# Kernel tuning notes

Hardware: AMD Instinct MI355X
Metric: run time of the kernel (lower is better)

## Reference

```python
import jax, jax.numpy as jnp
import numpy as np

ROWS, COLS, CH = 16, 16, 3
HID, HEADS, BLEN = 512, 8, 128
NUM_POINTS = ROWS * COLS            # 256
SEQ = ROWS * COLS * CH              # 768
NF = 256
L = 6
EPS = 1e-6


def setup_inputs() -> dict:
    key = jax.random.key(0)
    ks = jax.random.split(key, 16)
    w = 0.02  # keep logits in a sane range
    return {
        "X": jax.random.uniform(ks[0], (16, CH, ROWS, COLS), jnp.float32),
        "embed_table": jax.random.normal(ks[1], (NUM_POINTS * CH, HID), jnp.float32) * w,
        "Wq": jax.random.normal(ks[2], (L, HID, HID), jnp.float32) * w,
        "Wk": jax.random.normal(ks[3], (L, HID, HID), jnp.float32) * w,
        "Wv": jax.random.normal(ks[4], (L, HID, HID), jnp.float32) * w,
        "Wo": jax.random.normal(ks[5], (L, HID, HID), jnp.float32) * w,
        "ln1_g": jnp.ones((L, HID), jnp.float32),
        "ln1_b": jnp.zeros((L, HID), jnp.float32),
        "W1": jax.random.normal(ks[6], (L, HID, 4 * HID), jnp.float32) * w,
        "b1": jnp.zeros((L, 4 * HID), jnp.float32),
        "W2": jax.random.normal(ks[7], (L, 4 * HID, HID), jnp.float32) * w,
        "b2": jnp.zeros((L, HID), jnp.float32),
        "ln2_g": jnp.ones((L, HID), jnp.float32),
        "ln2_b": jnp.zeros((L, HID), jnp.float32),
        "proj_W": jax.random.normal(ks[8], (HID * SEQ, NF), jnp.float32) * w,
        "out_ln_g": jnp.ones((NF,), jnp.float32),
        "out_ln_b": jnp.zeros((NF,), jnp.float32),
    }


def _ln(x, g, b):
    m = jnp.mean(x, axis=-1, keepdims=True)
    v = jnp.mean(jnp.square(x - m), axis=-1, keepdims=True)
    return (x - m) * jax.lax.rsqrt(v + EPS) * g + b


def _timing_signal(x4):
    # x4: [B, ROWS, COLS*CH, HID]; 2 spatial dims
    nts = HID // 4
    inv = jnp.exp(jnp.arange(nts, dtype=jnp.float32) * (-np.log(10000.0) / (nts - 1)))
    def sig(length, prepad, postpad):
        pos = jnp.arange(length, dtype=jnp.float32)
        st = pos[:, None] * inv[None, :]
        s = jnp.concatenate([jnp.sin(st), jnp.cos(st)], axis=1)  # [len, 2*nts]
        return jnp.pad(s, ((0, 0), (prepad, postpad)))
    s0 = sig(x4.shape[1], 0, HID - 2 * nts)          # dim 0 (rows)
    s1 = sig(x4.shape[2], 2 * nts, 0)                # dim 1 (cols*ch)
    return x4 + s0[None, :, None, :] + s1[None, None, :, :]


def _local_attn(x, wq, wk, wv, wo):
    B, S, _ = x.shape
    dh = HID // HEADS
    def heads(w):
        return (x @ w).reshape(B, S, HEADS, dh).transpose(0, 2, 1, 3)
    q = heads(wq) * (dh ** -0.5)
    k = heads(wk)
    v = heads(wv)
    nb = S // BLEN  # S is a multiple of BLEN here (768/128=6), so no padding
    neg = jnp.float32(-1e9)
    bias1 = neg * jnp.triu(jnp.ones((BLEN, BLEN), jnp.float32), 1)
    logits1 = jnp.einsum('bhkd,bhqd->bhqk', k[:, :, :BLEN], q[:, :, :BLEN]) + bias1
    first = jax.nn.softmax(logits1, axis=-1) @ v[:, :, :BLEN]  # [B,H,BLEN,dh]
    qb = q.reshape(B, HEADS, nb, BLEN, dh)
    kb = k.reshape(B, HEADS, nb, BLEN, dh)
    vb = v.reshape(B, HEADS, nb, BLEN, dh)
    lk = jnp.concatenate([kb[:, :, :-1], kb[:, :, 1:]], axis=3)  # [B,H,nb-1,2B,dh]
    lv = jnp.concatenate([vb[:, :, :-1], vb[:, :, 1:]], axis=3)
    tq = qb[:, :, 1:]
    bias2 = neg * jnp.triu(jnp.ones((BLEN, 2 * BLEN), jnp.float32), BLEN + 1)
    logits2 = jnp.einsum('bhnkd,bhnqd->bhnqk', lk, tq) + bias2
    tail = jnp.einsum('bhnqk,bhnkd->bhnqd', jax.nn.softmax(logits2, axis=-1), lv)
    tail = tail.reshape(B, HEADS, (nb - 1) * BLEN, dh)
    out = jnp.concatenate([first, tail], axis=2)  # [B,H,S,dh]
    out = out.transpose(0, 2, 1, 3).reshape(B, S, HID)
    return out @ wo


def reference(X, embed_table, Wq, Wk, Wv, Wo, ln1_g, ln1_b, W1, b1, W2, b2,
              ln2_g, ln2_b, proj_W, out_ln_g, out_ln_b):
    B = X.shape[0]
    # [B,C,H,W] -> [B,H,W,C] -> [B,H,W*C]
    x = X.transpose(0, 2, 3, 1).reshape(B, ROWS, COLS * CH)
    idx = (x * (NUM_POINTS - 1)).astype(jnp.int32)
    chan_add = jnp.tile(jnp.arange(CH, dtype=jnp.int32) * NUM_POINTS, COLS)  # [W*C]
    idx = idx + chan_add[None, None, :]
    e = embed_table[idx] * (HID ** 0.5)             # [B,H,W*C,HID]
    # shift_and_pad over flattened spatial dims
    flat = e.reshape(B, SEQ, HID)
    flat = jnp.pad(flat[:, :-1], ((0, 0), (1, 0), (0, 0)))
    e = flat.reshape(B, ROWS, COLS * CH, HID)
    e = _timing_signal(e)
    h = e.reshape(B, SEQ, HID)
    for i in range(L):
        y = _local_attn(h, Wq[i], Wk[i], Wv[i], Wo[i])
        h = _ln(y + h, ln1_g[i], ln1_b[i])
        y = jax.nn.gelu(h @ W1[i] + b1[i], approximate=False) @ W2[i] + b2[i]
        h = _ln(y + h, ln2_g[i], ln2_b[i])
    out = h.reshape(B, SEQ * HID) @ proj_W
    out = jax.nn.gelu(out, approximate=False)
    return _ln(out, out_ln_g, out_ln_b)
```

## Files before the change

### kernel.cpp

```cpp
#include <hip/hip_runtime.h>
#include <cstddef>

typedef __bf16 bf16;
typedef bf16 bf16x4 __attribute__((ext_vector_type(4)));
typedef bf16 bf16x8 __attribute__((ext_vector_type(8)));
typedef float f32x4 __attribute__((ext_vector_type(4)));

#define NLAYER 6
#define HIDD 512
#define SEQL 768
#define NBATCH 16
#define MROWS 12288
#define QKVS 1536

__device__ __forceinline__ void gll16(const void* g, void* l) {
  __builtin_amdgcn_global_load_lds((const __attribute__((address_space(1))) void*)g,
                                   (__attribute__((address_space(3))) void*)l, 16, 0, 0);
}

__device__ __forceinline__ float gelu_f(float v) {
  return 0.5f * v * (1.0f + erff(v * 0.7071067811865475f));
}

#define VMC8 asm volatile("s_waitcnt vmcnt(8)" ::: "memory");
#define VMC4 asm volatile("s_waitcnt vmcnt(4)" ::: "memory");
#define VMC0 asm volatile("s_waitcnt vmcnt(0)" ::: "memory");

__global__ __launch_bounds__(256) void prep(
    const float* __restrict__ X, const float* __restrict__ ET,
    const float* __restrict__ Wq, const float* __restrict__ Wk,
    const float* __restrict__ Wv, const float* __restrict__ Wo,
    const float* __restrict__ W1, const float* __restrict__ W2,
    const float* __restrict__ ln1g, const float* __restrict__ ln1b,
    const float* __restrict__ ln2g, const float* __restrict__ ln2b,
    bf16* __restrict__ Wqkvt, bf16* __restrict__ Wot,
    bf16* __restrict__ W1t, bf16* __restrict__ W2t,
    float* __restrict__ vQg, float* __restrict__ vQb,
    float* __restrict__ vW1g, float* __restrict__ vW1b,
    bf16* __restrict__ Zg2) {
  const int bx = blockIdx.x;
  const int t = threadIdx.x;
  if (bx < 18432) {
    const int l = bx / 3072, idx = bx % 3072;
    const float* src;
    bf16* dst;
    int K, N, kb, nb;
    if (idx < 1024) {
      const int which = idx >> 8, tile = idx & 255;
      nb = (tile & 15) * 32; kb = (tile >> 4) * 32; K = 512; N = 512;
      const float* s4[4] = {Wq, Wk, Wv, Wo};
      src = s4[which] + (size_t)l * 512 * 512;
      dst = (which < 3) ? (Wqkvt + (size_t)l * QKVS * 512 + (size_t)which * 512 * 512)
                        : (Wot + (size_t)l * 512 * 512);
    } else if (idx < 2048) {
      const int local = idx - 1024;
      nb = (local & 63) * 32; kb = (local >> 6) * 32; K = 512; N = 2048;
      src = W1 + (size_t)l * 512 * 2048; dst = W1t + (size_t)l * 512 * 2048;
    } else {
      const int local = idx - 2048;
      nb = (local & 15) * 32; kb = (local >> 4) * 32; K = 2048; N = 512;
      src = W2 + (size_t)l * 2048 * 512; dst = W2t + (size_t)l * 2048 * 512;
    }
    __shared__ float tile[32 * 33];
#pragma unroll
    for (int i = 0; i < 4; ++i) {
      int lin = i * 256 + t, r = lin >> 5, c = lin & 31;
      tile[r * 33 + c] = src[(size_t)(kb + r) * N + nb + c];
    }
    __syncthreads();
#pragma unroll
    for (int i = 0; i < 4; ++i) {
      int lin = i * 256 + t, r = lin >> 5, c = lin & 31;
      dst[(size_t)(nb + r) * K + kb + c] = (bf16)tile[c * 33 + r];
    }
    return;
  }
  if (bx < 18432 + 84) {
    const int i = bx - 18432;
    const int l = i / 14;
    const int c = (i % 14) * 256 + t;
    if (c < 1536) {
      float gv = 0.f, bv = 0.f;
      if (l > 0) {
        const float* gin = ln2g + (l - 1) * 512;
        const float* bin = ln2b + (l - 1) * 512;
        const float* W;
        int cc = c;
        if (c < 512) { W = Wq + (size_t)l * 512 * 512; }
        else if (c < 1024) { W = Wk + (size_t)l * 512 * 512; cc = c - 512; }
        else { W = Wv + (size_t)l * 512 * 512; cc = c - 1024; }
        for (int k = 0; k < 512; ++k) {
          const float w = W[(size_t)k * 512 + cc];
          gv += gin[k] * w;
          bv += bin[k] * w;
        }
      }
      vQg[l * 1536 + c] = gv;
      vQb[l * 1536 + c] = bv;
    } else {
      const int cc = c - 1536;
      const float* g1 = ln1g + l * 512;
      const float* b1 = ln1b + l * 512;
      const float* W = W1 + (size_t)l * 512 * 2048;
      float gv = 0.f, bv = 0.f;
      for (int k = 0; k < 512; ++k) {
        const float w = W[(size_t)k * 2048 + cc];
        gv += g1[k] * w;
        bv += b1[k] * w;
      }
      vW1g[l * 2048 + cc] = gv;
      vW1b[l * 2048 + cc] = bv;
    }
    return;
  }
  const int bs = (bx - 18516) * 2 + (t >> 7);
  const int tl = t & 127;
  const int s = bs % SEQL;
  const int b = bs / SEQL;
  const int r = s / 48, c = s % 48;
  float vals[4] = {0.f, 0.f, 0.f, 0.f};
  const int ssrc = s - 1;
  if (ssrc >= 0) {
    const int rs = ssrc / 48, c48 = ssrc % 48;
    const int col = c48 / 3, ch = c48 % 3;
    const float x = X[((b * 3 + ch) * 16 + rs) * 16 + col];
    const int idx = (int)(x * 255.0f) + ch * 256;
    const float sq = 22.62741699796952f;
#pragma unroll
    for (int i = 0; i < 4; ++i) vals[i] = ET[(size_t)idx * HIDD + tl + 128 * i] * sq;
  }
  const float Cc = -0.07252236513366286f;
#pragma unroll
  for (int i = 0; i < 4; ++i) {
    const int d = tl + 128 * i;
    float ts;
    if (d < 128)      ts = sinf((float)r * expf((float)d * Cc));
    else if (d < 256) ts = cosf((float)r * expf((float)(d - 128) * Cc));
    else if (d < 384) ts = sinf((float)c * expf((float)(d - 256) * Cc));
    else              ts = cosf((float)c * expf((float)(d - 384) * Cc));
    Zg2[(size_t)bs * HIDD + d] = (bf16)(vals[i] + ts);
  }
}

template <int EPI, bool L0, int KT>
__global__ __launch_bounds__(256) void gemm2p(const bf16* __restrict__ A,
                                              const bf16* __restrict__ Bt,
                                              bf16* __restrict__ C,
                                              bf16* __restrict__ vT,
                                              const float* __restrict__ pIn,
                                              const float* __restrict__ vg,
                                              const float* __restrict__ vb,
                                              const float* __restrict__ bias,
                                              int N) {
  constexpr int K = KT;
  constexpr int NI = K >> 5;
  __shared__ char sbuf[49152];
  __shared__ float rsL[128], rsmL[128];
  const int tid = threadIdx.x;
  const int lane = tid & 63, w = tid >> 6;
  const int wr = w >> 1, wc = w & 1;
  const int l15 = lane & 15, g = lane >> 4;
  const int m0 = blockIdx.y * 128, n0 = blockIdx.x * 128;
  f32x4 acc[4][4] = {};
  const int rr0 = tid >> 2, kc = tid & 3;
  const bf16* Ap0 = A + (size_t)(m0 + rr0) * K + kc * 8;
  const bf16* Ap1 = A + (size_t)(m0 + 64 + rr0) * K + kc * 8;
  const bf16* Bp0 = Bt + (size_t)(n0 + rr0) * K + kc * 8;
  const bf16* Bp1 = Bt + (size_t)(n0 + 64 + rr0) * K + kc * 8;

  auto STAGE = [&](int st, int kt) {
    char* base = sbuf + st * 16384;
    gll16(Ap0 + kt, base + tid * 16);
    gll16(Ap1 + kt, base + 4096 + tid * 16);
    gll16(Bp0 + kt, base + 8192 + tid * 16);
    gll16(Bp1 + kt, base + 12288 + tid * 16);
  };

  STAGE(0, 0);
  STAGE(1, 32);
#pragma unroll 3
  for (int it = 0; it < NI; ++it) {
    const int cur = it % 3;
    if (it + 2 < NI) {
      STAGE((it + 2) % 3, (it + 2) * 32);
      VMC8;
    } else if (it + 1 < NI) {
      VMC4;
    } else {
      VMC0;
    }
    __builtin_amdgcn_s_barrier();
    const char* base = sbuf + cur * 16384;
    bf16x8 af[4], bv[4];
#pragma unroll
    for (int i = 0; i < 4; ++i)
      af[i] = *(const bf16x8*)(base + ((wr * 64 + i * 16 + l15) * 32 + 8 * g) * 2);
#pragma unroll
    for (int i = 0; i < 4; ++i)
      bv[i] = *(const bf16x8*)(base + 8192 + ((wc * 64 + i * 16 + l15) * 32 + 8 * g) * 2);
#pragma unroll
    for (int mi = 0; mi < 4; ++mi)
#pragma unroll
      for (int ni = 0; ni < 4; ++ni)
        acc[mi][ni] = __builtin_amdgcn_mfma_f32_16x16x32_bf16(af[mi], bv[ni], acc[mi][ni], 0, 0, 0);
    __builtin_amdgcn_s_barrier();
  }

  if constexpr (!L0) {
    if (tid < 128) {
      const int row = m0 + tid;
      float s = 0.f, q = 0.f;
#pragma unroll
      for (int j = 0; j < 8; ++j) {
        s += pIn[(size_t)j * MROWS + row];
        q += pIn[(size_t)(8 + j) * MROWS + row];
      }
      const float mean = s * (1.0f / 512.0f);
      const float var = q * (1.0f / 512.0f) - mean * mean;
      const float rs = rsqrtf(var + 1e-6f);
      rsL[tid] = rs;
      rsmL[tid] = rs * mean;
    }
    __syncthreads();
  }

  const bool VPATH = (EPI == 0) && (n0 >= 1024);
#pragma unroll
  for (int mi = 0; mi < 4; ++mi)
#pragma unroll
    for (int nf = 0; nf < 4; ++nf) {
      const int lr = wr * 64 + mi * 16 + 4 * g;
      const int row = m0 + lr;
      const int col = n0 + wc * 64 + nf * 16 + l15;
      float vgc = 0.f, vbc = 0.f, bc = 0.f;
      if constexpr (!L0) { vgc = vg[col]; vbc = vb[col]; }
      if constexpr (EPI == 1) bc = bias[col];
      float val[4];
#pragma unroll
      for (int r = 0; r < 4; ++r) {
        float a = acc[mi][nf][r];
        float v;
        if constexpr (L0) v = a;
        else v = rsL[lr + r] * a - rsmL[lr + r] * vgc + vbc;
        if constexpr (EPI == 1) v = gelu_f(v + bc);
        val[r] = v;
      }
      if (VPATH) {
        const int cv = col - 1024, hh = cv >> 6, dd = cv & 63;
        const int b = row / SEQL, s = row % SEQL;
        bf16x4 q4;
#pragma unroll
        for (int r = 0; r < 4; ++r) q4[r] = (bf16)val[r];
        *(bf16x4*)&vT[(size_t)((b * 8 + hh) * 64 + dd) * SEQL + s] = q4;
      } else {
#pragma unroll
        for (int r = 0; r < 4; ++r)
          C[(size_t)(row + r) * N + col] = (bf16)val[r];
      }
    }
}

template <int EPI, int KT>
__global__ __launch_bounds__(256) void gemm_fuse(const bf16* __restrict__ A,
                                                 const bf16* __restrict__ Bt,
                                                 const bf16* __restrict__ zgIn,
                                                 const float* __restrict__ pIn,
                                                 const float* __restrict__ vg_in,
                                                 const float* __restrict__ vb_in,
                                                 const float* __restrict__ extra_b,
                                                 const float* __restrict__ g_out,
                                                 bf16* __restrict__ zgOut,
                                                 float* __restrict__ pOut) {
  constexpr int N = 512;
  constexpr int K = KT;
  constexpr int NI = K >> 5;
  __shared__ char sbuf[49152];
  __shared__ float rsL[128], rsmL[128];
  const int tid = threadIdx.x;
  const int lane = tid & 63, w = tid >> 6;
  const int wr = w >> 1, wc = w & 1;
  const int l15 = lane & 15, g = lane >> 4;
  const int m0 = blockIdx.y * 128, n0 = blockIdx.x * 128;
  f32x4 acc[4][4] = {};
  const int rr0 = tid >> 2, kc = tid & 3;
  const bf16* Ap0 = A + (size_t)(m0 + rr0) * K + kc * 8;
  const bf16* Ap1 = A + (size_t)(m0 + 64 + rr0) * K + kc * 8;
  const bf16* Bp0 = Bt + (size_t)(n0 + rr0) * K + kc * 8;
  const bf16* Bp1 = Bt + (size_t)(n0 + 64 + rr0) * K + kc * 8;

  auto STAGE = [&](int st, int kt) {
    char* base = sbuf + st * 16384;
    gll16(Ap0 + kt, base + tid * 16);
    gll16(Ap1 + kt, base + 4096 + tid * 16);
    gll16(Bp0 + kt, base + 8192 + tid * 16);
    gll16(Bp1 + kt, base + 12288 + tid * 16);
  };

  STAGE(0, 0);
  STAGE(1, 32);
#pragma unroll 3
  for (int it = 0; it < NI; ++it) {
    const int cur = it % 3;
    if (it + 2 < NI) {
      STAGE((it + 2) % 3, (it + 2) * 32);
      VMC8;
    } else if (it + 1 < NI) {
      VMC4;
    } else {
      VMC0;
    }
    __builtin_amdgcn_s_barrier();
    const char* base = sbuf + cur * 16384;
    bf16x8 af[4], bv[4];
#pragma unroll
    for (int i = 0; i < 4; ++i)
      af[i] = *(const bf16x8*)(base + ((wr * 64 + i * 16 + l15) * 32 + 8 * g) * 2);
#pragma unroll
    for (int i = 0; i < 4; ++i)
      bv[i] = *(const bf16x8*)(base + 8192 + ((wc * 64 + i * 16 + l15) * 32 + 8 * g) * 2);
#pragma unroll
    for (int mi = 0; mi < 4; ++mi)
#pragma unroll
      for (int ni = 0; ni < 4; ++ni)
        acc[mi][ni] = __builtin_amdgcn_mfma_f32_16x16x32_bf16(af[mi], bv[ni], acc[mi][ni], 0, 0, 0);
    __builtin_amdgcn_s_barrier();
  }

  bf16* ztile = (bf16*)sbuf;
#pragma unroll
  for (int j = 0; j < 8; ++j) {
    const int row = j * 16 + (tid >> 4);
    const bf16* gsrc = zgIn + (size_t)(m0 + row) * N + n0 + (tid & 15) * 8;
    gll16(gsrc, sbuf + j * 4096 + tid * 16);
  }

  if constexpr (EPI != 0) {
    if (tid < 128) {
      const int row = m0 + tid;
      float s = 0.f, q = 0.f;
#pragma unroll
      for (int j = 0; j < 8; ++j) {
        s += pIn[(size_t)j * MROWS + row];
        q += pIn[(size_t)(8 + j) * MROWS + row];
      }
      const float mean = s * (1.0f / 512.0f);
      const float var = q * (1.0f / 512.0f) - mean * mean;
      const float rs = rsqrtf(var + 1e-6f);
      rsL[tid] = rs;
      rsmL[tid] = rs * mean;
    }
  }
  VMC0;
  __syncthreads();

  const int nb = n0 >> 7;
  float vgc[4], vbc[4], go[4], eb[4];
#pragma unroll
  for (int ni = 0; ni < 4; ++ni) {
    const int col = n0 + wc * 64 + ni * 16 + l15;
    if constexpr (EPI != 0) { vgc[ni] = vg_in[col]; vbc[ni] = vb_in[col]; }
    go[ni] = g_out[col];
    if constexpr (EPI == 2) eb[ni] = extra_b[col];
  }
#pragma unroll
  for (int mi = 0; mi < 4; ++mi) {
#pragma unroll
    for (int rr = 0; rr < 4; ++rr) {
      const int lr = wr * 64 + mi * 16 + 4 * g + rr;
      const int row = m0 + lr;
      float s = 0.f, q = 0.f;
#pragma unroll
      for (int ni = 0; ni < 4; ++ni) {
        const int lc = wc * 64 + ni * 16 + l15;
        const float zgv = (float)ztile[lr * 128 + lc];
        float hprev;
        if constexpr (EPI == 0) hprev = zgv;
        else hprev = rsL[lr] * zgv - rsmL[lr] * vgc[ni] + vbc[ni];
        float z = acc[mi][ni][rr] + hprev;
        if constexpr (EPI == 2) z += eb[ni];
        s += z;
        q += z * z;
        ztile[lr * 128 + lc] = (bf16)(z * go[ni]);
      }
      s += __shfl_xor(s, 1); s += __shfl_xor(s, 2); s += __shfl_xor(s, 4); s += __shfl_xor(s, 8);
      q += __shfl_xor(q, 1); q += __shfl_xor(q, 2); q += __shfl_xor(q, 4); q += __shfl_xor(q, 8);
      if (l15 == 0) {
        pOut[(size_t)(nb * 2 + wc) * MROWS + row] = s;
        pOut[(size_t)(8 + nb * 2 + wc) * MROWS + row] = q;
      }
    }
  }
  __syncthreads();
#pragma unroll
  for (int i = 0; i < 8; ++i) {
    const int id = i * 256 + tid;
    const int row = id >> 4, c16 = id & 15;
    bf16x8 v = *(const bf16x8*)&ztile[row * 128 + c16 * 8];
    *(bf16x8*)&zgOut[(size_t)(m0 + row) * N + n0 + c16 * 8] = v;
  }
}

template <bool FIRST>
__device__ __forceinline__ void attn_body(int n, int h, int b, const bf16* __restrict__ Qb,
                                          const bf16* __restrict__ Kb,
                                          const bf16* __restrict__ Vt,
                                          bf16* __restrict__ O, bf16* __restrict__ P) {
  constexpr int NF = FIRST ? 8 : 16;
  constexpr int KC = FIRST ? 4 : 8;
  const int tid = threadIdx.x, w = tid >> 6, lane = tid & 63;
  const int l15 = lane & 15, g = lane >> 4;
  const int keybase = FIRST ? 0 : (n - 1) * 128;
  const int qbase = n * 128;
  const bf16* qrow = Qb + (size_t)(b * SEQL + qbase + w * 16 + l15) * QKVS + h * 64;
  bf16x8 qf0 = *(const bf16x8*)(qrow + 8 * g);
  bf16x8 qf1 = *(const bf16x8*)(qrow + 32 + 8 * g);
  f32x4 S[NF];
#pragma unroll
  for (int nf = 0; nf < NF; ++nf) S[nf] = f32x4{0.f, 0.f, 0.f, 0.f};
#pragma unroll
  for (int nf = 0; nf < NF; ++nf) {
    const bf16* krow = Kb + (size_t)(b * SEQL + keybase + nf * 16 + l15) * QKVS + h * 64;
    bf16x8 kf0 = *(const bf16x8*)(krow + 8 * g);
    bf16x8 kf1 = *(const bf16x8*)(krow + 32 + 8 * g);
    S[nf] = __builtin_amdgcn_mfma_f32_16x16x32_bf16(qf0, kf0, S[nf], 0, 0, 0);
    S[nf] = __builtin_amdgcn_mfma_f32_16x16x32_bf16(qf1, kf1, S[nf], 0, 0, 0);
  }
#pragma unroll
  for (int rr = 0; rr < 4; ++rr) {
    const int qloc = w * 16 + 4 * g + rr;
    float mx = -3.0e38f;
#pragma unroll
    for (int nf = 0; nf < NF; ++nf) {
      const int key = nf * 16 + l15;
      const bool valid = FIRST ? (key <= qloc) : (key <= qloc + 128);
      float v = valid ? S[nf][rr] * 0.125f : -1.0e9f;
      S[nf][rr] = v;
      mx = fmaxf(mx, v);
    }
    mx = fmaxf(mx, __shfl_xor(mx, 1));
    mx = fmaxf(mx, __shfl_xor(mx, 2));
    mx = fmaxf(mx, __shfl_xor(mx, 4));
    mx = fmaxf(mx, __shfl_xor(mx, 8));
    float sden = 0.f;
#pragma unroll
    for (int nf = 0; nf < NF; ++nf) {
      float e = expf(S[nf][rr] - mx);
      S[nf][rr] = e;
      sden += e;
    }
    sden += __shfl_xor(sden, 1);
    sden += __shfl_xor(sden, 2);
    sden += __shfl_xor(sden, 4);
    sden += __shfl_xor(sden, 8);
    const float rcp = 1.0f / sden;
#pragma unroll
    for (int nf = 0; nf < NF; ++nf)
      P[w * 4096 + (4 * g + rr) * 256 + nf * 16 + l15] = (bf16)(S[nf][rr] * rcp);
  }
  f32x4 Oacc[4];
#pragma unroll
  for (int i = 0; i < 4; ++i) Oacc[i] = f32x4{0.f, 0.f, 0.f, 0.f};
#pragma unroll
  for (int kc = 0; kc < KC; ++kc) {
    bf16x8 pa = *(const bf16x8*)&P[w * 4096 + l15 * 256 + kc * 32 + 8 * g];
#pragma unroll
    for (int nf = 0; nf < 4; ++nf) {
      const bf16* vrow = Vt + (size_t)((b * 8 + h) * 64 + nf * 16 + l15) * SEQL +
                         keybase + kc * 32 + 8 * g;
      bf16x8 vf = *(const bf16x8*)vrow;
      Oacc[nf] = __builtin_amdgcn_mfma_f32_16x16x32_bf16(pa, vf, Oacc[nf], 0, 0, 0);
    }
  }
  bf16* Ow = P + w * 4096;
#pragma unroll
  for (int nf = 0; nf < 4; ++nf)
#pragma unroll
    for (int rr = 0; rr < 4; ++rr)
      Ow[(4 * g + rr) * 68 + nf * 16 + l15] = (bf16)Oacc[nf][rr];
#pragma unroll
  for (int i = 0; i < 2; ++i) {
    const int id = i * 64 + lane;
    const int row = id >> 3, c8 = id & 7;
    bf16x8 v = *(const bf16x8*)&Ow[row * 68 + c8 * 8];
    *(bf16x8*)&O[(size_t)(b * SEQL + qbase + w * 16 + row) * HIDD + h * 64 + c8 * 8] = v;
  }
}

__global__ __launch_bounds__(512) void attn_all(const bf16* __restrict__ Qb,
                                                const bf16* __restrict__ Kb,
                                                const bf16* __restrict__ Vt,
                                                bf16* __restrict__ O) {
  __shared__ bf16 P[8 * 4096];
  const int n = blockIdx.x, h = blockIdx.y, b = blockIdx.z;
  if (n == 0)
    attn_body<true>(0, h, b, Qb, Kb, Vt, O, P);
  else
    attn_body<false>(n, h, b, Qb, Kb, Vt, O, P);
}

__global__ __launch_bounds__(256) void proj_partial(const bf16* __restrict__ zg2,
                                                    const float* __restrict__ pSQ2,
                                                    const float* __restrict__ g5,
                                                    const float* __restrict__ b5,
                                                    const float* __restrict__ W,
                                                    float* __restrict__ part) {
  const int kc = blockIdx.x;
  const int t = threadIdx.x;
  __shared__ float Al[512 * 20];
  __shared__ float gld[512], bld[512], rsP[16], rsmP[16];
  gld[t] = g5[t]; gld[t + 256] = g5[t + 256];
  bld[t] = b5[t]; bld[t + 256] = b5[t + 256];
  if (t < 16) {
    const int row = t * SEQL + kc;
    float s = 0.f, q = 0.f;
#pragma unroll
    for (int j = 0; j < 8; ++j) {
      s += pSQ2[(size_t)j * MROWS + row];
      q += pSQ2[(size_t)(8 + j) * MROWS + row];
    }
    const float mean = s * (1.0f / 512.0f);
    const float var = q * (1.0f / 512.0f) - mean * mean;
    const float rs = rsqrtf(var + 1e-6f);
    rsP[t] = rs;
    rsmP[t] = rs * mean;
  }
  __syncthreads();
#pragma unroll
  for (int i = 0; i < 32; ++i) {
    int lin = i * 256 + t, m = lin >> 9, kk = lin & 511;
    const int row = m * SEQL + kc;
    Al[kk * 20 + m] = rsP[m] * (float)zg2[(size_t)row * 512 + kk] - rsmP[m] * gld[kk] + bld[kk];
  }
  __syncthreads();
  const size_t k0 = (size_t)kc * 512;
  float acc[16] = {};
  for (int kk = 0; kk < 512; ++kk) {
    const float wv = W[(k0 + kk) * 256 + t];
    const f32x4* a = (const f32x4*)&Al[kk * 20];
#pragma unroll
    for (int j = 0; j < 4; ++j) {
      f32x4 av = a[j];
      acc[j * 4 + 0] += av[0] * wv;
      acc[j * 4 + 1] += av[1] * wv;
      acc[j * 4 + 2] += av[2] * wv;
      acc[j * 4 + 3] += av[3] * wv;
    }
  }
#pragma unroll
  for (int m = 0; m < 16; ++m) part[(size_t)kc * 4096 + m * 256 + t] = acc[m];
}

__global__ __launch_bounds__(256) void proj_reduce1(const float* __restrict__ part,
                                                    float* __restrict__ part2) {
  const int i = blockIdx.x * 256 + threadIdx.x;
  const int cb = blockIdx.y;
  float s = 0.f;
  for (int c = cb * 64; c < cb * 64 + 64; ++c) s += part[(size_t)c * 4096 + i];
  part2[(size_t)cb * 4096 + i] = s;
}

__global__ __launch_bounds__(256) void proj_final(const float* __restrict__ part2,
                                                  const float* __restrict__ g,
                                                  const float* __restrict__ bt,
                                                  float* __restrict__ out) {
  const int row = blockIdx.x, t = threadIdx.x;
  float v = 0.f;
#pragma unroll
  for (int c = 0; c < 12; ++c) v += part2[(size_t)c * 4096 + row * 256 + t];
  const float x = gelu_f(v);
  __shared__ float red[256];
  red[t] = x;
  __syncthreads();
  for (int off = 128; off > 0; off >>= 1) {
    if (t < off) red[t] += red[t + off];
    __syncthreads();
  }
  const float mean = red[0] * (1.0f / 256.0f);
  __syncthreads();
  const float dx = x - mean;
  red[t] = dx * dx;
  __syncthreads();
  for (int off = 128; off > 0; off >>= 1) {
    if (t < off) red[t] += red[t + off];
    __syncthreads();
  }
  const float var = red[0] * (1.0f / 256.0f);
  const float rs = rsqrtf(var + 1e-6f);
  out[row * 256 + t] = dx * rs * g[t] + bt[t];
}

extern "C" void kernel_launch(void* const* d_in, const int* in_sizes, int n_in,
                              void* d_out, int out_size, void* d_ws, size_t ws_size,
                              hipStream_t stream) {
  const float* X = (const float*)d_in[0];
  const float* ET = (const float*)d_in[1];
  const float* Wq = (const float*)d_in[2];
  const float* Wk = (const float*)d_in[3];
  const float* Wv = (const float*)d_in[4];
  const float* Wo = (const float*)d_in[5];
  const float* ln1g = (const float*)d_in[6];
  const float* ln1b = (const float*)d_in[7];
  const float* W1 = (const float*)d_in[8];
  const float* b1 = (const float*)d_in[9];
  const float* W2 = (const float*)d_in[10];
  const float* b2 = (const float*)d_in[11];
  const float* ln2g = (const float*)d_in[12];
  const float* ln2b = (const float*)d_in[13];
  const float* PW = (const float*)d_in[14];
  const float* og = (const float*)d_in[15];
  const float* obv = (const float*)d_in[16];
  float* out = (float*)d_out;

  char* p = (char*)d_ws;
  auto alloc = [&](size_t bytes) {
    char* r = p;
    p += (bytes + 255) & ~(size_t)255;
    return r;
  };
  bf16* Wqkvt = (bf16*)alloc((size_t)NLAYER * QKVS * 512 * 2);
  bf16* Wot = (bf16*)alloc((size_t)NLAYER * 512 * 512 * 2);
  bf16* W1t = (bf16*)alloc((size_t)NLAYER * 512 * 2048 * 2);
  bf16* W2t = (bf16*)alloc((size_t)NLAYER * 512 * 2048 * 2);
  float* vQg = (float*)alloc((size_t)NLAYER * QKVS * 4);
  float* vQb = (float*)alloc((size_t)NLAYER * QKVS * 4);
  float* vW1g = (float*)alloc((size_t)NLAYER * 2048 * 4);
  float* vW1b = (float*)alloc((size_t)NLAYER * 2048 * 4);
  bf16* zg2 = (bf16*)alloc((size_t)MROWS * HIDD * 2);
  bf16* zg1 = (bf16*)alloc((size_t)MROWS * HIDD * 2);
  float* pSQ1 = (float*)alloc((size_t)16 * MROWS * 4);
  float* pSQ2 = (float*)alloc((size_t)16 * MROWS * 4);
  bf16* qkvB = (bf16*)alloc((size_t)MROWS * QKVS * 2);
  bf16* vT = (bf16*)alloc((size_t)MROWS * HIDD * 2);
  bf16* aO = (bf16*)alloc((size_t)MROWS * HIDD * 2);
  bf16* mid = (bf16*)alloc((size_t)MROWS * 2048 * 2);
  float* part = (float*)alloc((size_t)768 * 4096 * 4);
  float* part2 = (float*)alloc((size_t)12 * 4096 * 4);
  (void)ws_size; (void)n_in; (void)in_sizes; (void)out_size;

  prep<<<24660, 256, 0, stream>>>(X, ET, Wq, Wk, Wv, Wo, W1, W2, ln1g, ln1b, ln2g, ln2b,
                                  Wqkvt, Wot, W1t, W2t, vQg, vQb, vW1g, vW1b, zg2);

  for (int i = 0; i < NLAYER; ++i) {
    const bf16* WqkvL = Wqkvt + (size_t)i * QKVS * 512;
    const bf16* WoL = Wot + (size_t)i * 512 * 512;
    const bf16* W1L = W1t + (size_t)i * 512 * 2048;
    const bf16* W2L = W2t + (size_t)i * 512 * 2048;
    if (i == 0)
      gemm2p<0, true, 512><<<dim3(12, 96), 256, 0, stream>>>(zg2, WqkvL, qkvB, vT, pSQ2,
                                                             vQg, vQb, nullptr, QKVS);
    else
      gemm2p<0, false, 512><<<dim3(12, 96), 256, 0, stream>>>(zg2, WqkvL, qkvB, vT, pSQ2,
                                                              vQg + i * QKVS, vQb + i * QKVS,
                                                              nullptr, QKVS);
    attn_all<<<dim3(6, 8, 16), 512, 0, stream>>>(qkvB, qkvB + 512, vT, aO);
    if (i == 0)
      gemm_fuse<0, 512><<<dim3(4, 96), 256, 0, stream>>>(aO, WoL, zg2, nullptr, nullptr,
                                                         nullptr, nullptr, ln1g, zg1, pSQ1);
    else
      gemm_fuse<1, 512><<<dim3(4, 96), 256, 0, stream>>>(aO, WoL, zg2, pSQ2,
                                                         ln2g + (i - 1) * 512,
                                                         ln2b + (i - 1) * 512, nullptr,
                                                         ln1g + i * 512, zg1, pSQ1);
    gemm2p<1, false, 512><<<dim3(16, 96), 256, 0, stream>>>(zg1, W1L, mid, nullptr, pSQ1,
                                                            vW1g + i * 2048, vW1b + i * 2048,
                                                            b1 + i * 2048, 2048);
    gemm_fuse<2, 2048><<<dim3(4, 96), 256, 0, stream>>>(mid, W2L, zg1, pSQ1, ln1g + i * 512,
                                                        ln1b + i * 512, b2 + i * 512,
                                                        ln2g + i * 512, zg2, pSQ2);
  }

  proj_partial<<<768, 256, 0, stream>>>(zg2, pSQ2, ln2g + 5 * 512, ln2b + 5 * 512, PW, part);
  proj_reduce1<<<dim3(16, 12), 256, 0, stream>>>(part, part2);
  proj_final<<<16, 256, 0, stream>>>(part2, og, obv, out);
}
```

Before: 1.434 ms.

## Stage K and V tiles in swizzled LDS for local attention

Attention blocks now bulk-load the K and V tiles for their key window into LDS with global_load_lds, using an XOR swizzle. All 8 waves then read those tiles from LDS instead of each wave fetching the same K/V rows from global memory. Probabilities are kept in registers and written to LDS one 32-key chunk at a time, and O is stored directly from the accumulators. Launch bounds now request 4 waves per SIMD. Shared memory per block grows to about 74KB, which may limit occupancy, and the direct O stores are narrower.

```diff
diff --git a/kernel.cpp b/kernel.cpp
--- a/kernel.cpp
+++ b/kernel.cpp
@@ -400,28 +400,55 @@
   }
 }
 
-template <bool FIRST>
-__device__ __forceinline__ void attn_body(int n, int h, int b, const bf16* __restrict__ Qb,
+template <int NKEY>
+__device__ __forceinline__ void attn_body(int n, int h, int b,
+                                          const bf16* __restrict__ Qb,
                                           const bf16* __restrict__ Kb,
                                           const bf16* __restrict__ Vt,
-                                          bf16* __restrict__ O, bf16* __restrict__ P) {
-  constexpr int NF = FIRST ? 8 : 16;
-  constexpr int KC = FIRST ? 4 : 8;
+                                          bf16* __restrict__ O,
+                                          bf16* __restrict__ Ks,
+                                          bf16* __restrict__ Vs,
+                                          bf16* __restrict__ Pc) {
+  constexpr int NF = NKEY / 16;
+  constexpr int KC = NKEY / 32;
+  constexpr int VG = NKEY / 8;
   const int tid = threadIdx.x, w = tid >> 6, lane = tid & 63;
   const int l15 = lane & 15, g = lane >> 4;
-  const int keybase = FIRST ? 0 : (n - 1) * 128;
+  const int keybase = (NKEY == 128) ? 0 : (n - 1) * 128;
   const int qbase = n * 128;
+
+#pragma unroll
+  for (int p = 0; p < NKEY / 64; ++p) {
+    const int j = p * 512 + tid;
+    const int row = j >> 3, lg = j & 7;
+    const int pg = lg ^ (row & 7);
+    gll16(Kb + (size_t)(b * SEQL + keybase + row) * QKVS + h * 64 + pg * 8, Ks + j * 8);
+  }
+#pragma unroll
+  for (int p = 0; p < NKEY / 64; ++p) {
+    const int j = p * 512 + tid;
+    const int row = j / VG, lg = j % VG;
+    const int pg = lg ^ (row & (VG - 1));
+    gll16(Vt + (size_t)((b * 8 + h) * 64 + row) * SEQL + keybase + pg * 8, Vs + j * 8);
+  }
+
   const bf16* qrow = Qb + (size_t)(b * SEQL + qbase + w * 16 + l15) * QKVS + h * 64;
   bf16x8 qf0 = *(const bf16x8*)(qrow + 8 * g);
   bf16x8 qf1 = *(const bf16x8*)(qrow + 32 + 8 * g);
+
+  VMC0;
+  __syncthreads();
+
   f32x4 S[NF];
 #pragma unroll
   for (int nf = 0; nf < NF; ++nf) S[nf] = f32x4{0.f, 0.f, 0.f, 0.f};
 #pragma unroll
   for (int nf = 0; nf < NF; ++nf) {
-    const bf16* krow = Kb + (size_t)(b * SEQL + keybase + nf * 16 + l15) * QKVS + h * 64;
-    bf16x8 kf0 = *(const bf16x8*)(krow + 8 * g);
-    bf16x8 kf1 = *(const bf16x8*)(krow + 32 + 8 * g);
+    const int krow = nf * 16 + l15;
+    const int pg0 = g ^ (krow & 7);
+    const int pg1 = (g + 4) ^ (krow & 7);
+    bf16x8 kf0 = *(const bf16x8*)&Ks[krow * 64 + pg0 * 8];
+    bf16x8 kf1 = *(const bf16x8*)&Ks[krow * 64 + pg1 * 8];
     S[nf] = __builtin_amdgcn_mfma_f32_16x16x32_bf16(qf0, kf0, S[nf], 0, 0, 0);
     S[nf] = __builtin_amdgcn_mfma_f32_16x16x32_bf16(qf1, kf1, S[nf], 0, 0, 0);
   }
@@ -432,7 +459,7 @@
 #pragma unroll
     for (int nf = 0; nf < NF; ++nf) {
       const int key = nf * 16 + l15;
-      const bool valid = FIRST ? (key <= qloc) : (key <= qloc + 128);
+      const bool valid = (NKEY == 128) ? (key <= qloc) : (key <= qloc + 128);
       float v = valid ? S[nf][rr] * 0.125f : -1.0e9f;
       S[nf][rr] = v;
       mx = fmaxf(mx, v);
@@ -454,48 +481,49 @@
     sden += __shfl_xor(sden, 8);
     const float rcp = 1.0f / sden;
 #pragma unroll
-    for (int nf = 0; nf < NF; ++nf)
-      P[w * 4096 + (4 * g + rr) * 256 + nf * 16 + l15] = (bf16)(S[nf][rr] * rcp);
-  }
+    for (int nf = 0; nf < NF; ++nf) S[nf][rr] *= rcp;
+  }
+
+  bf16* pcw = Pc + w * 640;
   f32x4 Oacc[4];
 #pragma unroll
   for (int i = 0; i < 4; ++i) Oacc[i] = f32x4{0.f, 0.f, 0.f, 0.f};
 #pragma unroll
   for (int kc = 0; kc < KC; ++kc) {
-    bf16x8 pa = *(const bf16x8*)&P[w * 4096 + l15 * 256 + kc * 32 + 8 * g];
+#pragma unroll
+    for (int rr = 0; rr < 4; ++rr) {
+      pcw[(4 * g + rr) * 40 + l15] = (bf16)S[2 * kc][rr];
+      pcw[(4 * g + rr) * 40 + 16 + l15] = (bf16)S[2 * kc + 1][rr];
+    }
+    bf16x8 pa = *(const bf16x8*)&pcw[l15 * 40 + 8 * g];
 #pragma unroll
     for (int nf = 0; nf < 4; ++nf) {
-      const bf16* vrow = Vt + (size_t)((b * 8 + h) * 64 + nf * 16 + l15) * SEQL +
-                         keybase + kc * 32 + 8 * g;
-      bf16x8 vf = *(const bf16x8*)vrow;
+      const int vrow = nf * 16 + l15;
+      const int pg = (kc * 4 + g) ^ (vrow & (VG - 1));
+      bf16x8 vf = *(const bf16x8*)&Vs[vrow * NKEY + pg * 8];
       Oacc[nf] = __builtin_amdgcn_mfma_f32_16x16x32_bf16(pa, vf, Oacc[nf], 0, 0, 0);
     }
   }
-  bf16* Ow = P + w * 4096;
 #pragma unroll
   for (int nf = 0; nf < 4; ++nf)
 #pragma unroll
     for (int rr = 0; rr < 4; ++rr)
-      Ow[(4 * g + rr) * 68 + nf * 16 + l15] = (bf16)Oacc[nf][rr];
-#pragma unroll
-  for (int i = 0; i < 2; ++i) {
-    const int id = i * 64 + lane;
-    const int row = id >> 3, c8 = id & 7;
-    bf16x8 v = *(const bf16x8*)&Ow[row * 68 + c8 * 8];
-    *(bf16x8*)&O[(size_t)(b * SEQL + qbase + w * 16 + row) * HIDD + h * 64 + c8 * 8] = v;
-  }
-}
-
-__global__ __launch_bounds__(512) void attn_all(const bf16* __restrict__ Qb,
-                                                const bf16* __restrict__ Kb,
-                                                const bf16* __restrict__ Vt,
-                                                bf16* __restrict__ O) {
-  __shared__ bf16 P[8 * 4096];
+      O[(size_t)(b * SEQL + qbase + w * 16 + 4 * g + rr) * HIDD + h * 64 + nf * 16 + l15] =
+          (bf16)Oacc[nf][rr];
+}
+
+__global__ __launch_bounds__(512, 4) void attn_all(const bf16* __restrict__ Qb,
+                                                   const bf16* __restrict__ Kb,
+                                                   const bf16* __restrict__ Vt,
+                                                   bf16* __restrict__ O) {
+  __shared__ bf16 Ks[256 * 64];
+  __shared__ bf16 Vs[64 * 256];
+  __shared__ bf16 Pc[8 * 640];
   const int n = blockIdx.x, h = blockIdx.y, b = blockIdx.z;
   if (n == 0)
-    attn_body<true>(0, h, b, Qb, Kb, Vt, O, P);
+    attn_body<128>(0, h, b, Qb, Kb, Vt, O, Ks, Vs, Pc);
   else
-    attn_body<false>(n, h, b, Qb, Kb, Vt, O, P);
+    attn_body<256>(n, h, b, Qb, Kb, Vt, O, Ks, Vs, Pc);
 }
 
 __global__ __launch_bounds__(256) void proj_partial(const bf16* __restrict__ zg2,
```

Result: faster. 1.246 ms (median of 2 runs) (-13.1%).
